# Optimization experiments

Measured on AMD Instinct MI355X. Metric: run time of the kernel, lower is better.

## Reference

```python
import jax, jax.numpy as jnp
import numpy as np
from jax import lax

# ---- dims / config (see init_kwargs) ----
M_IMG, N_PCD, C = 1008, 1024, 256     # coarse img nodes (24*32+12*16+6*8), coarse pcd nodes, feat dim
NI_F, NP_F = 76800, 30000             # fine img pixels (240*320), fine pcd points
KI, KP = 64, 64                       # knn patch sizes
NUM_CORR, TOPK = 256, 3               # coarse matching params
COARSE_THR, FINE_THR = 0.0, 0.0       # similarity thresholds (lowered for random data)


def _norm(x):
    return x / (jnp.linalg.norm(x, axis=-1, keepdims=True) + 1e-8)


def setup_inputs() -> dict:
    key = jax.random.key(0)
    ks = jax.random.split(key, 7)
    return {
        "img_feats_c": _norm(jax.random.normal(ks[0], (M_IMG, C), jnp.float32)),
        "pcd_feats_c": _norm(jax.random.normal(ks[1], (N_PCD, C), jnp.float32)),
        "img_feats_f": _norm(jax.random.normal(ks[2], (NI_F, C), jnp.float32)),
        "pcd_feats_f": _norm(jax.random.normal(ks[3], (NP_F, C), jnp.float32)),
        "img_node_masks": jnp.ones((M_IMG,), bool),
        "pcd_node_masks": jnp.ones((N_PCD,), bool),
        "img_node_knn_indices": jax.random.randint(ks[4], (M_IMG, KI), 0, NI_F),
        "pcd_node_knn_indices": jax.random.randint(ks[5], (N_PCD, KP), 0, NP_F),
        "pcd_node_knn_masks": jax.random.uniform(ks[6], (N_PCD, KP)) > 0.1,
    }


def _coarse_match(img_feats_c, pcd_feats_c, img_masks, pcd_masks):
    # SuperPointMatchingMutualTopk: cosine sim + mutual top-k + global top NUM_CORR
    sim = img_feats_c @ pcd_feats_c.T                              # [M, N] (feats normalized)
    valid = img_masks[:, None] & pcd_masks[None, :]
    sim_m = jnp.where(valid, sim, -jnp.inf)
    row_kth = lax.top_k(sim_m, TOPK)[0][:, -1:]                    # kth-largest per row [M,1]
    col_kth = lax.top_k(sim_m.T, TOPK)[0][:, -1:].T                # kth-largest per col [1,N]
    mutual = (sim_m >= row_kth) & (sim_m >= col_kth) & (sim_m > COARSE_THR)
    flat = jnp.where(mutual, sim_m, -jnp.inf).ravel()
    vals, flat_idx = lax.top_k(flat, NUM_CORR)                     # fixed-size selection
    img_idx = flat_idx // N_PCD
    pcd_idx = flat_idx % N_PCD
    corr_valid = jnp.isfinite(vals)
    return img_idx, pcd_idx, corr_valid


def reference(img_feats_c, pcd_feats_c, img_feats_f, pcd_feats_f,
              img_node_masks, pcd_node_masks,
              img_node_knn_indices, pcd_node_knn_indices, pcd_node_knn_masks):
    # ---- coarse matching ----
    img_idx, pcd_idx, corr_valid = _coarse_match(
        img_feats_c, pcd_feats_c, img_node_masks, pcd_node_masks)

    # ---- fine matching: knn gather + pairwise cosine + mutual top-1 ----
    pcd_padded = jnp.concatenate([pcd_feats_f, jnp.zeros_like(pcd_feats_f[:1])], axis=0)
    img_knn_idx = img_node_knn_indices[img_idx]                    # [Ci, KI]
    pcd_knn_idx = pcd_node_knn_indices[pcd_idx]                    # [Ci, KP]
    pcd_knn_msk = pcd_node_knn_masks[pcd_idx]                      # [Ci, KP]
    img_knn_feats = img_feats_f[img_knn_idx]                       # [Ci, KI, C]
    pcd_knn_feats = pcd_padded[pcd_knn_idx]                        # [Ci, KP, C]

    sim = jnp.einsum('bic,bjc->bij', img_knn_feats, pcd_knn_feats) # [Ci, KI, KP]
    m3 = corr_valid[:, None, None] & pcd_knn_msk[:, None, :]
    sim = jnp.where(m3, sim, -jnp.inf)

    row_best = jnp.argmax(sim, axis=2)                             # [Ci, KI]
    row_val = jnp.max(sim, axis=2)
    col_best = jnp.argmax(sim, axis=1)                             # [Ci, KP]
    back = jnp.take_along_axis(col_best, row_best, axis=1)         # [Ci, KI]
    sel = (back == jnp.arange(KI)[None, :]) & jnp.isfinite(row_val) & (row_val > FINE_THR)

    img_corr = img_knn_idx.reshape(-1)                             # [Ci*KI]
    pcd_corr = jnp.take_along_axis(pcd_knn_idx, row_best, axis=1).reshape(-1)
    sel = sel.reshape(-1)
    # sentinel for unselected pairs -> sorts last
    img_corr = jnp.where(sel, img_corr, NI_F)
    pcd_corr = jnp.where(sel, pcd_corr, NP_F)

    # ---- dedup (torch.unique on img*Npf+pcd) via lexsort + first-occurrence mask ----
    order = jnp.lexsort((pcd_corr, img_corr))
    ic, pc = img_corr[order], pcd_corr[order]
    first = jnp.concatenate([jnp.array([True]),
                             (ic[1:] != ic[:-1]) | (pc[1:] != pc[:-1])])
    valid = first & (ic < NI_F)

    ic_s = jnp.clip(ic, 0, NI_F - 1)
    pc_s = jnp.clip(pc, 0, NP_F - 1)
    corr_scores = jnp.sum(img_feats_f[ic_s] * pcd_feats_f[pc_s], axis=1)
    corr_scores = corr_scores * valid.astype(corr_scores.dtype)    # masked scores [Ci*KI]
    return corr_scores
```

## Files before the change

### kernel.cpp

```cpp
#include <hip/hip_runtime.h>
#include <hip/hip_bf16.h>

#define M_IMG 1008
#define N_PCD 1024
#define CDIM  256
#define NI_F  76800
#define NP_F  30000
#define KI    64
#define KP    64
#define NUM_CORR 256
#define NPAIR (NUM_CORR * KI)
#define CAND_CAP 4096
#define KEY_MOD 30001u
#define SENT_KEY (76800u * 30001u + 30000u)

#define NCHUNK 21
#define NEG_INF (-__builtin_inff())

__device__ __forceinline__ bool mask_val(const void* p, int i, int is_u8) {
    return is_u8 ? (((const unsigned char*)p)[i] != 0)
                 : (((const int*)p)[i] != 0);
}

__global__ void detect_bool_kernel(const unsigned int* __restrict__ p,
                                   int* __restrict__ flag) {
    __shared__ int s_cnt;
    if (threadIdx.x == 0) s_cnt = 0;
    __syncthreads();
    unsigned int x = p[blockIdx.x * 256 + threadIdx.x];
    if (x & 0xFFFFFF00u) atomicAdd(&s_cnt, 1);
    __syncthreads();
    if (threadIdx.x == 0 && s_cnt != 0) atomicAdd(flag, 1);
}


__global__ void coarse_sim_kernel(const float* __restrict__ A,
                                  const float* __restrict__ B,
                                  const void* __restrict__ maskA,
                                  const void* __restrict__ maskB,
                                  const int* __restrict__ flag,
                                  float* __restrict__ sim) {
    __shared__ __align__(16) float s_a[32][36];
    __shared__ __align__(16) float s_b[32][68];
    const int is_u8 = (*flag != 0);
    const int m0 = blockIdx.y * 32, n0 = blockIdx.x * 64;
    const int tid = threadIdx.x;
    const int tx = tid & 15, ty = tid >> 4;
    const int c_lane = tid & 31;
    const int r_base = tid >> 5;

    const float* pa[4];
    const float* pb[8];
#pragma unroll
    for (int k = 0; k < 4; k++) {
        int m = m0 + r_base + 8 * k;
        pa[k] = A + (size_t)(m < M_IMG ? m : 0) * CDIM + c_lane;
    }
#pragma unroll
    for (int k = 0; k < 8; k++)
        pb[k] = B + (size_t)(n0 + r_base + 8 * k) * CDIM + c_lane;

    float ra[4], rb[8];
#pragma unroll
    for (int k = 0; k < 4; k++) ra[k] = pa[k][0];
#pragma unroll
    for (int k = 0; k < 8; k++) rb[k] = pb[k][0];
#pragma unroll
    for (int k = 0; k < 4; k++) s_a[c_lane][r_base + 8 * k] = ra[k];
#pragma unroll
    for (int k = 0; k < 8; k++) s_b[c_lane][r_base + 8 * k] = rb[k];
    __syncthreads();

    float acc[2][4];
#pragma unroll
    for (int r = 0; r < 2; r++)
#pragma unroll
        for (int j = 0; j < 4; j++) acc[r][j] = 0.f;

    for (int cit = 0; cit < 8; cit++) {
        if (cit < 7) {
            const int cc = (cit + 1) * 32;
#pragma unroll
            for (int k = 0; k < 4; k++) ra[k] = pa[k][cc];
#pragma unroll
            for (int k = 0; k < 8; k++) rb[k] = pb[k][cc];
        }
#pragma unroll 8
        for (int c = 0; c < 32; c++) {
            float2 av = *(const float2*)&s_a[c][ty * 2];
            float4 bv = *(const float4*)&s_b[c][tx * 4];
            float ar[2] = {av.x, av.y};
            float br[4] = {bv.x, bv.y, bv.z, bv.w};
#pragma unroll
            for (int r = 0; r < 2; r++)
#pragma unroll
                for (int j = 0; j < 4; j++) acc[r][j] += ar[r] * br[j];
        }
        __syncthreads();
        if (cit < 7) {
#pragma unroll
            for (int k = 0; k < 4; k++) s_a[c_lane][r_base + 8 * k] = ra[k];
#pragma unroll
            for (int k = 0; k < 8; k++) s_b[c_lane][r_base + 8 * k] = rb[k];
            __syncthreads();
        }
    }
#pragma unroll
    for (int r = 0; r < 2; r++) {
        int m = m0 + ty * 2 + r;
        if (m < M_IMG) {
            bool ma = mask_val(maskA, m, is_u8);
#pragma unroll
            for (int j = 0; j < 4; j++) {
                int n = n0 + tx * 4 + j;
                bool ok = ma && mask_val(maskB, n, is_u8);
                sim[m * N_PCD + n] = ok ? acc[r][j] : NEG_INF;
            }
        }
    }
}

__device__ __forceinline__ void top3_insert(float v, float& t0, float& t1, float& t2) {
    if (v > t0) { t2 = t1; t1 = t0; t0 = v; }
    else if (v > t1) { t2 = t1; t1 = v; }
    else if (v > t2) { t2 = v; }
}

__device__ __forceinline__ void top3_merge(float a0, float a1, float a2,
                                           float b0, float b1, float b2,
                                           float& x0, float& x1, float& x2) {
    if (a0 >= b0) {
        x0 = a0;
        if (a1 >= b0) { x1 = a1; x2 = (a2 >= b0) ? a2 : b0; }
        else          { x1 = b0; x2 = (a1 >= b1) ? a1 : b1; }
    } else {
        x0 = b0;
        if (b1 >= a0) { x1 = b1; x2 = (b2 >= a0) ? b2 : a0; }
        else          { x1 = a0; x2 = (b1 >= a1) ? b1 : a1; }
    }
}

__global__ void kth_kernel(const float* __restrict__ sim,
                           float* __restrict__ row_kth,
                           float* __restrict__ colp) {
    __shared__ float st[256][3];
    const int tid = threadIdx.x;
    if (blockIdx.x < M_IMG) {
        const float* r = sim + (size_t)blockIdx.x * N_PCD;
        float t0 = NEG_INF, t1 = NEG_INF, t2 = NEG_INF;
#pragma unroll
        for (int e = 0; e < 4; e++) top3_insert(r[e * 256 + tid], t0, t1, t2);
        st[tid][0] = t0; st[tid][1] = t1; st[tid][2] = t2;
        __syncthreads();
        for (int s = 128; s > 0; s >>= 1) {
            if (tid < s) {
                float x0, x1, x2;
                top3_merge(st[tid][0], st[tid][1], st[tid][2],
                           st[tid + s][0], st[tid + s][1], st[tid + s][2],
                           x0, x1, x2);
                st[tid][0] = x0; st[tid][1] = x1; st[tid][2] = x2;
            }
            __syncthreads();
        }
        if (tid == 0) row_kth[blockIdx.x] = st[0][2];
    } else {
        const int b = blockIdx.x - M_IMG;
        const int bx = b & 15, by = b >> 4;
        const int c = tid & 63, rr = tid >> 6;
        const int col = bx * 64 + c;
        const int r0 = by * 48;
        float t0 = NEG_INF, t1 = NEG_INF, t2 = NEG_INF;
#pragma unroll
        for (int k = 0; k < 12; k++) {
            float v = sim[(size_t)(r0 + rr + 4 * k) * N_PCD + col];
            top3_insert(v, t0, t1, t2);
        }
        st[tid][0] = t0; st[tid][1] = t1; st[tid][2] = t2;
        __syncthreads();
        if (tid < 128) {
            float x0, x1, x2;
            top3_merge(st[tid][0], st[tid][1], st[tid][2],
                       st[tid + 128][0], st[tid + 128][1], st[tid + 128][2],
                       x0, x1, x2);
            st[tid][0] = x0; st[tid][1] = x1; st[tid][2] = x2;
        }
        __syncthreads();
        if (tid < 64) {
            float x0, x1, x2;
            top3_merge(st[tid][0], st[tid][1], st[tid][2],
                       st[tid + 64][0], st[tid + 64][1], st[tid + 64][2],
                       x0, x1, x2);
            const int base = by * N_PCD + col;
            colp[base] = x0;
            colp[NCHUNK * N_PCD + base] = x1;
            colp[2 * NCHUNK * N_PCD + base] = x2;
        }
    }
}

__global__ void col_merge_kernel(const float* __restrict__ colp,
                                 float* __restrict__ col_kth) {
    const int col = blockIdx.x * 256 + threadIdx.x;
    float t0 = colp[col];
    float t1 = colp[NCHUNK * N_PCD + col];
    float t2 = colp[2 * NCHUNK * N_PCD + col];
#pragma unroll
    for (int ch = 1; ch < NCHUNK; ch++) {
        float b0 = colp[ch * N_PCD + col];
        float b1 = colp[NCHUNK * N_PCD + ch * N_PCD + col];
        float b2 = colp[2 * NCHUNK * N_PCD + ch * N_PCD + col];
        float x0, x1, x2;
        top3_merge(t0, t1, t2, b0, b1, b2, x0, x1, x2);
        t0 = x0; t1 = x1; t2 = x2;
    }
    col_kth[col] = t2;
}

__global__ void compact_kernel(const float* __restrict__ sim,
                               const float* __restrict__ row_kth,
                               const float* __restrict__ col_kth,
                               unsigned long long* __restrict__ cand,
                               int* __restrict__ count) {
    int g = blockIdx.x * 256 + threadIdx.x;
    if (g >= M_IMG * N_PCD) return;
    int m = g >> 10, n = g & 1023;
    float v = sim[g];
    if (v > 0.f && v >= row_kth[m] && v >= col_kth[n]) {
        int pos = atomicAdd(count, 1);
        if (pos < CAND_CAP) {
            unsigned int u = __float_as_uint(v);
            unsigned int mono = (u & 0x80000000u) ? ~u : (u | 0x80000000u);
            cand[pos] = ((unsigned long long)(~mono) << 32) | (unsigned int)g;
        }
    }
}

__global__ void cand_rank_kernel(const unsigned long long* __restrict__ cand,
                                 const int* __restrict__ count,
                                 unsigned int* __restrict__ cnt2) {
    __shared__ unsigned long long s_k[256];
    const int tid = threadIdx.x;
    int K = *count; if (K > CAND_CAP) K = CAND_CAP;
    const int j0 = blockIdx.y * 256;
    if (j0 >= K) return;
    int j = j0 + tid;
    s_k[tid] = (j < K) ? cand[j] : 0xFFFFFFFFFFFFFFFFull;
    __syncthreads();
    const int i = blockIdx.x * 256 + tid;
    if (i >= K) return;
    const unsigned long long my = cand[i];
    unsigned int less = 0;
#pragma unroll 8
    for (int t = 0; t < 256; t++) less += (s_k[t] < my);
    if (less) atomicAdd(&cnt2[i], less);
}

__global__ void cand_select_kernel(const unsigned long long* __restrict__ cand,
                                   const int* __restrict__ count,
                                   const unsigned int* __restrict__ cnt2,
                                   int* __restrict__ sel_idx,
                                   int* __restrict__ selK) {
    int K = *count; if (K > CAND_CAP) K = CAND_CAP;
    const int i = blockIdx.x * 256 + threadIdx.x;
    if (i == 0) *selK = (K < NUM_CORR) ? K : NUM_CORR;
    if (i < K) {
        unsigned int r = cnt2[i];
        if (r < NUM_CORR) sel_idx[r] = (int)(cand[i] & 0xFFFFFFFFull);
    }
}

__global__ void fine_kernel(const float* __restrict__ img_f,
                            const float* __restrict__ pcd_f,
                            const int* __restrict__ img_knn,
                            const int* __restrict__ pcd_knn,
                            const void* __restrict__ pcd_msk,
                            const int* __restrict__ flag,
                            const int* __restrict__ sel_idx,
                            const int* __restrict__ selK_ptr,
                            unsigned int* __restrict__ keys) {
    const int ci = blockIdx.x, tid = threadIdx.x;
    const int selK = *selK_ptr;
    if (ci >= selK) {
        if (tid < KI) keys[ci * KI + tid] = SENT_KEY;
        return;
    }
    __shared__ int s_ik[KI], s_pk[KP];
    __shared__ unsigned char s_mk[KP];
    __shared__ __align__(16) float s_a[32][68];
    __shared__ __align__(16) float s_b[32][68];
    __shared__ float s_sim[64][65];
    __shared__ int s_rb[64], s_cb[64];
    __shared__ float s_rv[64];

    int flat = sel_idx[ci];
    int gi = flat >> 10, pi = flat & 1023;
    if (tid < 64) {
        const int is_u8 = (*flag != 0);
        s_ik[tid] = img_knn[gi * KI + tid];
        s_pk[tid] = pcd_knn[pi * KP + tid];
        s_mk[tid] = mask_val(pcd_msk, pi * KP + tid, is_u8) ? 1 : 0;
    }
    __syncthreads();

    const int tx = tid & 15, tyy = tid >> 4;
    const int c_lane = tid & 31;
    const int r_base = tid >> 5;

    const float* pa[4];
    const float* pb[4];
#pragma unroll
    for (int k = 0; k < 4; k++) {
        pa[k] = img_f + (size_t)s_ik[r_base + 16 * k] * CDIM + c_lane;
        pb[k] = pcd_f + (size_t)s_pk[r_base + 16 * k] * CDIM + c_lane;
    }

    float ra[4], rb[4];
#pragma unroll
    for (int k = 0; k < 4; k++) { ra[k] = pa[k][0]; rb[k] = pb[k][0]; }
#pragma unroll
    for (int k = 0; k < 4; k++) {
        s_a[c_lane][r_base + 16 * k] = ra[k];
        s_b[c_lane][r_base + 16 * k] = rb[k];
    }
    __syncthreads();

    float acc[2][4];
#pragma unroll
    for (int r = 0; r < 2; r++)
#pragma unroll
        for (int j = 0; j < 4; j++) acc[r][j] = 0.f;

    for (int cit = 0; cit < 8; cit++) {
        if (cit < 7) {
            const int cc = (cit + 1) * 32;
#pragma unroll
            for (int k = 0; k < 4; k++) { ra[k] = pa[k][cc]; rb[k] = pb[k][cc]; }
        }
#pragma unroll 8
        for (int c = 0; c < 32; c++) {
            float2 av = *(const float2*)&s_a[c][tyy * 2];
            float4 bv = *(const float4*)&s_b[c][tx * 4];
            float ar[2] = {av.x, av.y};
            float br[4] = {bv.x, bv.y, bv.z, bv.w};
#pragma unroll
            for (int r = 0; r < 2; r++)
#pragma unroll
                for (int j = 0; j < 4; j++) acc[r][j] += ar[r] * br[j];
        }
        __syncthreads();
        if (cit < 7) {
#pragma unroll
            for (int k = 0; k < 4; k++) {
                s_a[c_lane][r_base + 16 * k] = ra[k];
                s_b[c_lane][r_base + 16 * k] = rb[k];
            }
            __syncthreads();
        }
    }
#pragma unroll
    for (int r = 0; r < 2; r++) {
        int row = tyy * 2 + r;
#pragma unroll
        for (int j = 0; j < 4; j++) {
            int kp = tx * 4 + j;
            s_sim[row][kp] = (s_mk[kp] != 0) ? acc[r][j] : NEG_INF;
        }
    }
    __syncthreads();

    if (tid < 64) {
        float best = NEG_INF; int bi = 0;
        for (int kp = 0; kp < 64; kp++) {
            float v = s_sim[tid][kp];
            if (v > best) { best = v; bi = kp; }
        }
        s_rb[tid] = bi; s_rv[tid] = best;
    } else if (tid < 128) {
        int kp = tid - 64;
        float best = NEG_INF; int bi = 0;
        for (int k2 = 0; k2 < 64; k2++) {
            float v = s_sim[k2][kp];
            if (v > best) { best = v; bi = k2; }
        }
        s_cb[kp] = bi;
    }
    __syncthreads();

    if (tid < 64) {
        int rb2 = s_rb[tid];
        float rv = s_rv[tid];
        bool sel = (s_cb[rb2] == tid) && (rv > 0.f);
        unsigned int key = sel
            ? ((unsigned int)s_ik[tid] * KEY_MOD + (unsigned int)s_pk[rb2])
            : SENT_KEY;
        keys[ci * KI + tid] = key;
    }
}

__global__ void rank_count_kernel(const unsigned int* __restrict__ keys,
                                  unsigned int* __restrict__ cnt) {
    __shared__ unsigned int s_k[256];
    const int tid = threadIdx.x;
    const int bi = blockIdx.x, bj = blockIdx.y;
    const int i = bi * 256 + tid;
    const unsigned int myKey = keys[i];
    s_k[tid] = keys[bj * 256 + tid];
    __syncthreads();

    unsigned int less = 0, eqb = 0;
    if (bj < bi) {
#pragma unroll 8
        for (int j = 0; j < 256; j++) {
            unsigned int k = s_k[j];
            less += (k < myKey);
            eqb += (k == myKey);
        }
    } else if (bj == bi) {
#pragma unroll 8
        for (int j = 0; j < 256; j++) {
            unsigned int k = s_k[j];
            less += (k < myKey);
            eqb += (k == myKey) & (j < tid);
        }
    } else {
#pragma unroll 8
        for (int j = 0; j < 256; j++) {
            unsigned int k = s_k[j];
            less += (k < myKey);
        }
    }
    atomicAdd(&cnt[i], (less << 16) | eqb);
}

__global__ void rank_out_kernel(const unsigned int* __restrict__ keys,
                                const unsigned int* __restrict__ cnt,
                                const float* __restrict__ img_f,
                                const float* __restrict__ pcd_f,
                                float* __restrict__ out) {
    const int i = blockIdx.x * 256 + threadIdx.x;
    const unsigned int myKey = keys[i];
    const unsigned int v = cnt[i];
    const int rank = (int)(v >> 16) + (int)(v & 0xFFFFu);
    unsigned int ic = myKey / KEY_MOD;
    unsigned int pc = myKey - ic * KEY_MOD;
    float score = 0.f;
    if ((v & 0xFFFFu) == 0 && ic < (unsigned)NI_F) {
        const float4* a = (const float4*)(img_f + (size_t)ic * CDIM);
        const float4* b = (const float4*)(pcd_f + (size_t)pc * CDIM);
        float s = 0.f;
#pragma unroll 8
        for (int c = 0; c < CDIM / 4; c++) {
            float4 x = a[c], y = b[c];
            s += x.x * y.x + x.y * y.y + x.z * y.z + x.w * y.w;
        }
        score = s;
    }
    out[rank] = score;
}

extern "C" void kernel_launch(void* const* d_in, const int* in_sizes, int n_in,
                              void* d_out, int out_size, void* d_ws, size_t ws_size,
                              hipStream_t stream) {
    const float* img_c = (const float*)d_in[0];
    const float* pcd_c = (const float*)d_in[1];
    const float* img_f = (const float*)d_in[2];
    const float* pcd_f = (const float*)d_in[3];
    const void* img_mask = d_in[4];
    const void* pcd_mask = d_in[5];
    const int* img_knn = (const int*)d_in[6];
    const int* pcd_knn = (const int*)d_in[7];
    const void* pcd_knn_msk = d_in[8];
    float* out = (float*)d_out;

    char* w = (char*)d_ws;
    size_t off = 0;
    float* sim = (float*)(w + off);            off += (size_t)M_IMG * N_PCD * 4;
    float* row_kth = (float*)(w + off);        off += M_IMG * 4;
    float* col_kth = (float*)(w + off);        off += N_PCD * 4;
    int* count = (int*)(w + off);              off += 4;
    int* selK = (int*)(w + off);               off += 4;
    int* boolflag = (int*)(w + off);           off += 4;
    off = (off + 7) & ~(size_t)7;
    unsigned long long* cand = (unsigned long long*)(w + off); off += CAND_CAP * 8;
    int* sel_idx = (int*)(w + off);            off += NUM_CORR * 4;
    unsigned int* keys = (unsigned int*)(w + off); off += NPAIR * 4;
    unsigned int* cnt = (unsigned int*)(w + off);  off += NPAIR * 4;
    unsigned int* cnt2 = (unsigned int*)(w + off); off += CAND_CAP * 4;
    float* colp = (float*)(w + off);           off += 3 * NCHUNK * N_PCD * 4;

    hipMemsetAsync(count, 0, 12, stream);
    hipMemsetAsync(cnt, 0, (NPAIR + CAND_CAP) * 4, stream);

    detect_bool_kernel<<<16, 256, 0, stream>>>((const unsigned int*)pcd_knn_msk, boolflag);
    coarse_sim_kernel<<<dim3(16, 32), 256, 0, stream>>>(img_c, pcd_c, img_mask, pcd_mask,
                                                        boolflag, sim);
    kth_kernel<<<M_IMG + 16 * NCHUNK, 256, 0, stream>>>(sim, row_kth, colp);
    col_merge_kernel<<<4, 256, 0, stream>>>(colp, col_kth);
    compact_kernel<<<(M_IMG * N_PCD) / 256, 256, 0, stream>>>(sim, row_kth, col_kth, cand, count);
    cand_rank_kernel<<<dim3(16, 16), 256, 0, stream>>>(cand, count, cnt2);
    cand_select_kernel<<<16, 256, 0, stream>>>(cand, count, cnt2, sel_idx, selK);
    fine_kernel<<<NUM_CORR, 512, 0, stream>>>(img_f, pcd_f, img_knn, pcd_knn, pcd_knn_msk,
                                              boolflag, sel_idx, selK, keys);
    rank_count_kernel<<<dim3(64, 64), 256, 0, stream>>>(keys, cnt);
    rank_out_kernel<<<NPAIR / 256, 256, 0, stream>>>(keys, cnt, img_f, pcd_f, out);
}
```

Baseline: 275.8 us.

## Collapse coarse/fine selection pipeline into fewer kernels with compacted keys

Removes the mask-detect kernel and memsets by folding bool detection and output zeroing into the coarse similarity kernel. Row top-3 now tracks indices, so the mutual check only scans 3 candidates per row instead of the whole similarity matrix. Column merge, candidate compaction and selection are fused into a single-block bitonic sort. Fine matches are compacted via an atomic counter, and one rank kernel computes ranks only over the valid keys, replacing the dense 16K x 16K rank count. The trade-off is a serial single-block sort stage and atomic ordering nondeterminism in the key list.

```diff
diff --git a/kernel.cpp b/kernel.cpp
--- a/kernel.cpp
+++ b/kernel.cpp
@@ -1,5 +1,4 @@
 #include <hip/hip_runtime.h>
-#include <hip/hip_bf16.h>
 
 #define M_IMG 1008
 #define N_PCD 1024
@@ -10,114 +9,14 @@
 #define KP    64
 #define NUM_CORR 256
 #define NPAIR (NUM_CORR * KI)
-#define CAND_CAP 4096
 #define KEY_MOD 30001u
-#define SENT_KEY (76800u * 30001u + 30000u)
-
 #define NCHUNK 21
+#define SORT_N 4096
 #define NEG_INF (-__builtin_inff())
 
 __device__ __forceinline__ bool mask_val(const void* p, int i, int is_u8) {
     return is_u8 ? (((const unsigned char*)p)[i] != 0)
                  : (((const int*)p)[i] != 0);
-}
-
-__global__ void detect_bool_kernel(const unsigned int* __restrict__ p,
-                                   int* __restrict__ flag) {
-    __shared__ int s_cnt;
-    if (threadIdx.x == 0) s_cnt = 0;
-    __syncthreads();
-    unsigned int x = p[blockIdx.x * 256 + threadIdx.x];
-    if (x & 0xFFFFFF00u) atomicAdd(&s_cnt, 1);
-    __syncthreads();
-    if (threadIdx.x == 0 && s_cnt != 0) atomicAdd(flag, 1);
-}
-
-
-__global__ void coarse_sim_kernel(const float* __restrict__ A,
-                                  const float* __restrict__ B,
-                                  const void* __restrict__ maskA,
-                                  const void* __restrict__ maskB,
-                                  const int* __restrict__ flag,
-                                  float* __restrict__ sim) {
-    __shared__ __align__(16) float s_a[32][36];
-    __shared__ __align__(16) float s_b[32][68];
-    const int is_u8 = (*flag != 0);
-    const int m0 = blockIdx.y * 32, n0 = blockIdx.x * 64;
-    const int tid = threadIdx.x;
-    const int tx = tid & 15, ty = tid >> 4;
-    const int c_lane = tid & 31;
-    const int r_base = tid >> 5;
-
-    const float* pa[4];
-    const float* pb[8];
-#pragma unroll
-    for (int k = 0; k < 4; k++) {
-        int m = m0 + r_base + 8 * k;
-        pa[k] = A + (size_t)(m < M_IMG ? m : 0) * CDIM + c_lane;
-    }
-#pragma unroll
-    for (int k = 0; k < 8; k++)
-        pb[k] = B + (size_t)(n0 + r_base + 8 * k) * CDIM + c_lane;
-
-    float ra[4], rb[8];
-#pragma unroll
-    for (int k = 0; k < 4; k++) ra[k] = pa[k][0];
-#pragma unroll
-    for (int k = 0; k < 8; k++) rb[k] = pb[k][0];
-#pragma unroll
-    for (int k = 0; k < 4; k++) s_a[c_lane][r_base + 8 * k] = ra[k];
-#pragma unroll
-    for (int k = 0; k < 8; k++) s_b[c_lane][r_base + 8 * k] = rb[k];
-    __syncthreads();
-
-    float acc[2][4];
-#pragma unroll
-    for (int r = 0; r < 2; r++)
-#pragma unroll
-        for (int j = 0; j < 4; j++) acc[r][j] = 0.f;
-
-    for (int cit = 0; cit < 8; cit++) {
-        if (cit < 7) {
-            const int cc = (cit + 1) * 32;
-#pragma unroll
-            for (int k = 0; k < 4; k++) ra[k] = pa[k][cc];
-#pragma unroll
-            for (int k = 0; k < 8; k++) rb[k] = pb[k][cc];
-        }
-#pragma unroll 8
-        for (int c = 0; c < 32; c++) {
-            float2 av = *(const float2*)&s_a[c][ty * 2];
-            float4 bv = *(const float4*)&s_b[c][tx * 4];
-            float ar[2] = {av.x, av.y};
-            float br[4] = {bv.x, bv.y, bv.z, bv.w};
-#pragma unroll
-            for (int r = 0; r < 2; r++)
-#pragma unroll
-                for (int j = 0; j < 4; j++) acc[r][j] += ar[r] * br[j];
-        }
-        __syncthreads();
-        if (cit < 7) {
-#pragma unroll
-            for (int k = 0; k < 4; k++) s_a[c_lane][r_base + 8 * k] = ra[k];
-#pragma unroll
-            for (int k = 0; k < 8; k++) s_b[c_lane][r_base + 8 * k] = rb[k];
-            __syncthreads();
-        }
-    }
-#pragma unroll
-    for (int r = 0; r < 2; r++) {
-        int m = m0 + ty * 2 + r;
-        if (m < M_IMG) {
-            bool ma = mask_val(maskA, m, is_u8);
-#pragma unroll
-            for (int j = 0; j < 4; j++) {
-                int n = n0 + tx * 4 + j;
-                bool ok = ma && mask_val(maskB, n, is_u8);
-                sim[m * N_PCD + n] = ok ? acc[r][j] : NEG_INF;
-            }
-        }
-    }
 }
 
 __device__ __forceinline__ void top3_insert(float v, float& t0, float& t1, float& t2) {
@@ -140,29 +39,146 @@
     }
 }
 
+__device__ __forceinline__ void t3i_insert(float v, int i,
+                                           float& v0, int& i0,
+                                           float& v1, int& i1,
+                                           float& v2, int& i2) {
+    if (v > v0) { v2 = v1; i2 = i1; v1 = v0; i1 = i0; v0 = v; i0 = i; }
+    else if (v > v1) { v2 = v1; i2 = i1; v1 = v; i1 = i; }
+    else if (v > v2) { v2 = v; i2 = i; }
+}
+
+__global__ void coarse_sim_kernel(const float* __restrict__ A,
+                                  const float* __restrict__ B,
+                                  const void* __restrict__ maskA,
+                                  const void* __restrict__ maskB,
+                                  const unsigned int* __restrict__ mskw,
+                                  float* __restrict__ sim,
+                                  float* __restrict__ out0,
+                                  int* __restrict__ nk) {
+    __shared__ __align__(16) float s_a[32][36];
+    __shared__ __align__(16) float s_b[32][68];
+    const int m0 = blockIdx.y * 32, n0 = blockIdx.x * 64;
+    const int tid = threadIdx.x;
+    const int tx = tid & 15, ty = tid >> 4;
+    const int c_lane = tid & 31;
+    const int r_base = tid >> 5;
+
+    const int bid = blockIdx.y * 16 + blockIdx.x;
+    if (tid < 32) out0[bid * 32 + tid] = 0.f;
+    if (bid == 0 && tid == 32) *nk = 0;
+
+    const bool hit = (mskw[tid] & 0xFFFFFF00u) != 0u;
+
+    const float* pa[4];
+    const float* pb[8];
+#pragma unroll
+    for (int k = 0; k < 4; k++) {
+        int m = m0 + r_base + 8 * k;
+        pa[k] = A + (size_t)(m < M_IMG ? m : 0) * CDIM + c_lane;
+    }
+#pragma unroll
+    for (int k = 0; k < 8; k++)
+        pb[k] = B + (size_t)(n0 + r_base + 8 * k) * CDIM + c_lane;
+
+    float ra[4], rb[8];
+#pragma unroll
+    for (int k = 0; k < 4; k++) ra[k] = pa[k][0];
+#pragma unroll
+    for (int k = 0; k < 8; k++) rb[k] = pb[k][0];
+#pragma unroll
+    for (int k = 0; k < 4; k++) s_a[c_lane][r_base + 8 * k] = ra[k];
+#pragma unroll
+    for (int k = 0; k < 8; k++) s_b[c_lane][r_base + 8 * k] = rb[k];
+    __syncthreads();
+
+    float acc[2][4];
+#pragma unroll
+    for (int r = 0; r < 2; r++)
+#pragma unroll
+        for (int j = 0; j < 4; j++) acc[r][j] = 0.f;
+
+    for (int cit = 0; cit < 8; cit++) {
+        if (cit < 7) {
+            const int cc = (cit + 1) * 32;
+#pragma unroll
+            for (int k = 0; k < 4; k++) ra[k] = pa[k][cc];
+#pragma unroll
+            for (int k = 0; k < 8; k++) rb[k] = pb[k][cc];
+        }
+#pragma unroll 8
+        for (int c = 0; c < 32; c++) {
+            float2 av = *(const float2*)&s_a[c][ty * 2];
+            float4 bv = *(const float4*)&s_b[c][tx * 4];
+            float ar[2] = {av.x, av.y};
+            float br[4] = {bv.x, bv.y, bv.z, bv.w};
+#pragma unroll
+            for (int r = 0; r < 2; r++)
+#pragma unroll
+                for (int j = 0; j < 4; j++) acc[r][j] += ar[r] * br[j];
+        }
+        __syncthreads();
+        if (cit < 7) {
+#pragma unroll
+            for (int k = 0; k < 4; k++) s_a[c_lane][r_base + 8 * k] = ra[k];
+#pragma unroll
+            for (int k = 0; k < 8; k++) s_b[c_lane][r_base + 8 * k] = rb[k];
+            __syncthreads();
+        }
+    }
+
+    const int is_u8 = __syncthreads_or(hit ? 1 : 0);
+#pragma unroll
+    for (int r = 0; r < 2; r++) {
+        int m = m0 + ty * 2 + r;
+        if (m < M_IMG) {
+            bool ma = mask_val(maskA, m, is_u8);
+#pragma unroll
+            for (int j = 0; j < 4; j++) {
+                int n = n0 + tx * 4 + j;
+                bool ok = ma && mask_val(maskB, n, is_u8);
+                sim[m * N_PCD + n] = ok ? acc[r][j] : NEG_INF;
+            }
+        }
+    }
+}
+
 __global__ void kth_kernel(const float* __restrict__ sim,
-                           float* __restrict__ row_kth,
+                           float* __restrict__ rowv3,
+                           int* __restrict__ rowi3,
                            float* __restrict__ colp) {
-    __shared__ float st[256][3];
+    __shared__ float sv[256][3];
+    __shared__ int   si[256][3];
     const int tid = threadIdx.x;
     if (blockIdx.x < M_IMG) {
         const float* r = sim + (size_t)blockIdx.x * N_PCD;
-        float t0 = NEG_INF, t1 = NEG_INF, t2 = NEG_INF;
-#pragma unroll
-        for (int e = 0; e < 4; e++) top3_insert(r[e * 256 + tid], t0, t1, t2);
-        st[tid][0] = t0; st[tid][1] = t1; st[tid][2] = t2;
+        float v0 = NEG_INF, v1 = NEG_INF, v2 = NEG_INF;
+        int i0 = 0, i1 = 0, i2 = 0;
+#pragma unroll
+        for (int e = 0; e < 4; e++) {
+            int c = e * 256 + tid;
+            t3i_insert(r[c], c, v0, i0, v1, i1, v2, i2);
+        }
+        sv[tid][0] = v0; sv[tid][1] = v1; sv[tid][2] = v2;
+        si[tid][0] = i0; si[tid][1] = i1; si[tid][2] = i2;
         __syncthreads();
         for (int s = 128; s > 0; s >>= 1) {
             if (tid < s) {
-                float x0, x1, x2;
-                top3_merge(st[tid][0], st[tid][1], st[tid][2],
-                           st[tid + s][0], st[tid + s][1], st[tid + s][2],
-                           x0, x1, x2);
-                st[tid][0] = x0; st[tid][1] = x1; st[tid][2] = x2;
+                float a0 = sv[tid][0], a1 = sv[tid][1], a2 = sv[tid][2];
+                int   j0 = si[tid][0], j1 = si[tid][1], j2 = si[tid][2];
+#pragma unroll
+                for (int k = 0; k < 3; k++)
+                    t3i_insert(sv[tid + s][k], si[tid + s][k],
+                               a0, j0, a1, j1, a2, j2);
+                sv[tid][0] = a0; sv[tid][1] = a1; sv[tid][2] = a2;
+                si[tid][0] = j0; si[tid][1] = j1; si[tid][2] = j2;
             }
             __syncthreads();
         }
-        if (tid == 0) row_kth[blockIdx.x] = st[0][2];
+        if (tid < 3) {
+            rowv3[blockIdx.x * 3 + tid] = sv[0][tid];
+            rowi3[blockIdx.x * 3 + tid] = si[0][tid];
+        }
     } else {
         const int b = blockIdx.x - M_IMG;
         const int bx = b & 15, by = b >> 4;
@@ -175,20 +191,20 @@
             float v = sim[(size_t)(r0 + rr + 4 * k) * N_PCD + col];
             top3_insert(v, t0, t1, t2);
         }
-        st[tid][0] = t0; st[tid][1] = t1; st[tid][2] = t2;
+        sv[tid][0] = t0; sv[tid][1] = t1; sv[tid][2] = t2;
         __syncthreads();
         if (tid < 128) {
             float x0, x1, x2;
-            top3_merge(st[tid][0], st[tid][1], st[tid][2],
-                       st[tid + 128][0], st[tid + 128][1], st[tid + 128][2],
+            top3_merge(sv[tid][0], sv[tid][1], sv[tid][2],
+                       sv[tid + 128][0], sv[tid + 128][1], sv[tid + 128][2],
                        x0, x1, x2);
-            st[tid][0] = x0; st[tid][1] = x1; st[tid][2] = x2;
+            sv[tid][0] = x0; sv[tid][1] = x1; sv[tid][2] = x2;
         }
         __syncthreads();
         if (tid < 64) {
             float x0, x1, x2;
-            top3_merge(st[tid][0], st[tid][1], st[tid][2],
-                       st[tid + 64][0], st[tid + 64][1], st[tid + 64][2],
+            top3_merge(sv[tid][0], sv[tid][1], sv[tid][2],
+                       sv[tid + 64][0], sv[tid + 64][1], sv[tid + 64][2],
                        x0, x1, x2);
             const int base = by * N_PCD + col;
             colp[base] = x0;
@@ -198,75 +214,68 @@
     }
 }
 
-__global__ void col_merge_kernel(const float* __restrict__ colp,
-                                 float* __restrict__ col_kth) {
-    const int col = blockIdx.x * 256 + threadIdx.x;
-    float t0 = colp[col];
-    float t1 = colp[NCHUNK * N_PCD + col];
-    float t2 = colp[2 * NCHUNK * N_PCD + col];
-#pragma unroll
-    for (int ch = 1; ch < NCHUNK; ch++) {
-        float b0 = colp[ch * N_PCD + col];
-        float b1 = colp[NCHUNK * N_PCD + ch * N_PCD + col];
-        float b2 = colp[2 * NCHUNK * N_PCD + ch * N_PCD + col];
-        float x0, x1, x2;
-        top3_merge(t0, t1, t2, b0, b1, b2, x0, x1, x2);
-        t0 = x0; t1 = x1; t2 = x2;
-    }
-    col_kth[col] = t2;
-}
-
-__global__ void compact_kernel(const float* __restrict__ sim,
-                               const float* __restrict__ row_kth,
-                               const float* __restrict__ col_kth,
-                               unsigned long long* __restrict__ cand,
-                               int* __restrict__ count) {
-    int g = blockIdx.x * 256 + threadIdx.x;
-    if (g >= M_IMG * N_PCD) return;
-    int m = g >> 10, n = g & 1023;
-    float v = sim[g];
-    if (v > 0.f && v >= row_kth[m] && v >= col_kth[n]) {
-        int pos = atomicAdd(count, 1);
-        if (pos < CAND_CAP) {
+__global__ __launch_bounds__(1024)
+void merge_select_kernel(const float* __restrict__ colp,
+                         const float* __restrict__ rowv3,
+                         const int* __restrict__ rowi3,
+                         int* __restrict__ sel_idx,
+                         int* __restrict__ selK) {
+    __shared__ float s_colk[N_PCD];
+    __shared__ __align__(16) unsigned long long s_cand[SORT_N];
+    __shared__ int s_cnt;
+    const int tid = threadIdx.x;
+
+    {
+        float t0 = colp[tid];
+        float t1 = colp[NCHUNK * N_PCD + tid];
+        float t2 = colp[2 * NCHUNK * N_PCD + tid];
+#pragma unroll 4
+        for (int ch = 1; ch < NCHUNK; ch++) {
+            float b0 = colp[ch * N_PCD + tid];
+            float b1 = colp[NCHUNK * N_PCD + ch * N_PCD + tid];
+            float b2 = colp[2 * NCHUNK * N_PCD + ch * N_PCD + tid];
+            float x0, x1, x2;
+            top3_merge(t0, t1, t2, b0, b1, b2, x0, x1, x2);
+            t0 = x0; t1 = x1; t2 = x2;
+        }
+        s_colk[tid] = t2;
+    }
+    if (tid == 0) s_cnt = 0;
+    for (int i = tid; i < SORT_N; i += 1024) s_cand[i] = ~0ULL;
+    __syncthreads();
+
+    for (int e = tid; e < M_IMG * 3; e += 1024) {
+        float v = rowv3[e];
+        int n = rowi3[e];
+        if (v > 0.f && v >= s_colk[n]) {
+            int m = e / 3;
+            int g = m * N_PCD + n;
             unsigned int u = __float_as_uint(v);
             unsigned int mono = (u & 0x80000000u) ? ~u : (u | 0x80000000u);
-            cand[pos] = ((unsigned long long)(~mono) << 32) | (unsigned int)g;
-        }
-    }
-}
-
-__global__ void cand_rank_kernel(const unsigned long long* __restrict__ cand,
-                                 const int* __restrict__ count,
-                                 unsigned int* __restrict__ cnt2) {
-    __shared__ unsigned long long s_k[256];
-    const int tid = threadIdx.x;
-    int K = *count; if (K > CAND_CAP) K = CAND_CAP;
-    const int j0 = blockIdx.y * 256;
-    if (j0 >= K) return;
-    int j = j0 + tid;
-    s_k[tid] = (j < K) ? cand[j] : 0xFFFFFFFFFFFFFFFFull;
-    __syncthreads();
-    const int i = blockIdx.x * 256 + tid;
-    if (i >= K) return;
-    const unsigned long long my = cand[i];
-    unsigned int less = 0;
-#pragma unroll 8
-    for (int t = 0; t < 256; t++) less += (s_k[t] < my);
-    if (less) atomicAdd(&cnt2[i], less);
-}
-
-__global__ void cand_select_kernel(const unsigned long long* __restrict__ cand,
-                                   const int* __restrict__ count,
-                                   const unsigned int* __restrict__ cnt2,
-                                   int* __restrict__ sel_idx,
-                                   int* __restrict__ selK) {
-    int K = *count; if (K > CAND_CAP) K = CAND_CAP;
-    const int i = blockIdx.x * 256 + threadIdx.x;
-    if (i == 0) *selK = (K < NUM_CORR) ? K : NUM_CORR;
-    if (i < K) {
-        unsigned int r = cnt2[i];
-        if (r < NUM_CORR) sel_idx[r] = (int)(cand[i] & 0xFFFFFFFFull);
-    }
+            int pos = atomicAdd(&s_cnt, 1);
+            s_cand[pos] = ((unsigned long long)(~mono) << 32) | (unsigned int)g;
+        }
+    }
+    __syncthreads();
+    int K = s_cnt;
+
+    for (int k = 2; k <= SORT_N; k <<= 1) {
+        for (int j = k >> 1; j > 0; j >>= 1) {
+            for (int i = tid; i < SORT_N; i += 1024) {
+                int ixj = i ^ j;
+                if (ixj > i) {
+                    bool up = ((i & k) == 0);
+                    unsigned long long a = s_cand[i], b = s_cand[ixj];
+                    if ((a > b) == up) { s_cand[i] = b; s_cand[ixj] = a; }
+                }
+            }
+            __syncthreads();
+        }
+    }
+
+    if (K > NUM_CORR) K = NUM_CORR;
+    if (tid == 0) *selK = K;
+    if (tid < K) sel_idx[tid] = (int)(s_cand[tid] & 0xFFFFFFFFu);
 }
 
 __global__ void fine_kernel(const float* __restrict__ img_f,
@@ -274,16 +283,13 @@
                             const int* __restrict__ img_knn,
                             const int* __restrict__ pcd_knn,
                             const void* __restrict__ pcd_msk,
-                            const int* __restrict__ flag,
+                            const unsigned int* __restrict__ mskw,
                             const int* __restrict__ sel_idx,
                             const int* __restrict__ selK_ptr,
-                            unsigned int* __restrict__ keys) {
+                            int* __restrict__ nk,
+                            unsigned int* __restrict__ ckeys) {
     const int ci = blockIdx.x, tid = threadIdx.x;
-    const int selK = *selK_ptr;
-    if (ci >= selK) {
-        if (tid < KI) keys[ci * KI + tid] = SENT_KEY;
-        return;
-    }
+    if (ci >= *selK_ptr) return;
     __shared__ int s_ik[KI], s_pk[KP];
     __shared__ unsigned char s_mk[KP];
     __shared__ __align__(16) float s_a[32][68];
@@ -292,15 +298,16 @@
     __shared__ int s_rb[64], s_cb[64];
     __shared__ float s_rv[64];
 
+    const bool hit = (mskw[tid & 255] & 0xFFFFFF00u) != 0u;
     int flat = sel_idx[ci];
     int gi = flat >> 10, pi = flat & 1023;
     if (tid < 64) {
-        const int is_u8 = (*flag != 0);
         s_ik[tid] = img_knn[gi * KI + tid];
         s_pk[tid] = pcd_knn[pi * KP + tid];
+    }
+    const int is_u8 = __syncthreads_or(hit ? 1 : 0);
+    if (tid < 64)
         s_mk[tid] = mask_val(pcd_msk, pi * KP + tid, is_u8) ? 1 : 0;
-    }
-    __syncthreads();
 
     const int tx = tid & 15, tyy = tid >> 4;
     const int c_lane = tid & 31;
@@ -389,62 +396,44 @@
     if (tid < 64) {
         int rb2 = s_rb[tid];
         float rv = s_rv[tid];
-        bool sel = (s_cb[rb2] == tid) && (rv > 0.f);
-        unsigned int key = sel
-            ? ((unsigned int)s_ik[tid] * KEY_MOD + (unsigned int)s_pk[rb2])
-            : SENT_KEY;
-        keys[ci * KI + tid] = key;
-    }
-}
-
-__global__ void rank_count_kernel(const unsigned int* __restrict__ keys,
-                                  unsigned int* __restrict__ cnt) {
+        if ((s_cb[rb2] == tid) && (rv > 0.f)) {
+            unsigned int key = (unsigned int)s_ik[tid] * KEY_MOD
+                             + (unsigned int)s_pk[rb2];
+            int pos = atomicAdd(nk, 1);
+            ckeys[pos] = key;
+        }
+    }
+}
+
+__global__ void rank_kernel(const unsigned int* __restrict__ ckeys,
+                            const int* __restrict__ nk,
+                            const float* __restrict__ img_f,
+                            const float* __restrict__ pcd_f,
+                            float* __restrict__ out) {
     __shared__ unsigned int s_k[256];
-    const int tid = threadIdx.x;
-    const int bi = blockIdx.x, bj = blockIdx.y;
+    const int K = *nk;
+    const int bi = blockIdx.x, tid = threadIdx.x;
+    if (bi * 256 >= K) return;
     const int i = bi * 256 + tid;
-    const unsigned int myKey = keys[i];
-    s_k[tid] = keys[bj * 256 + tid];
-    __syncthreads();
-
-    unsigned int less = 0, eqb = 0;
-    if (bj < bi) {
+    const unsigned int myKey = (i < K) ? ckeys[i] : 0xFFFFFFFFu;
+    int less = 0, eqb = 0;
+    const int nb = (K + 255) >> 8;
+    for (int bj = 0; bj < nb; bj++) {
+        const int j = bj * 256 + tid;
+        s_k[tid] = (j < K) ? ckeys[j] : 0xFFFFFFFFu;
+        __syncthreads();
+        const int jbase = bj * 256;
 #pragma unroll 8
-        for (int j = 0; j < 256; j++) {
-            unsigned int k = s_k[j];
+        for (int t = 0; t < 256; t++) {
+            unsigned int k = s_k[t];
             less += (k < myKey);
-            eqb += (k == myKey);
-        }
-    } else if (bj == bi) {
-#pragma unroll 8
-        for (int j = 0; j < 256; j++) {
-            unsigned int k = s_k[j];
-            less += (k < myKey);
-            eqb += (k == myKey) & (j < tid);
-        }
-    } else {
-#pragma unroll 8
-        for (int j = 0; j < 256; j++) {
-            unsigned int k = s_k[j];
-            less += (k < myKey);
-        }
-    }
-    atomicAdd(&cnt[i], (less << 16) | eqb);
-}
-
-__global__ void rank_out_kernel(const unsigned int* __restrict__ keys,
-                                const unsigned int* __restrict__ cnt,
-                                const float* __restrict__ img_f,
-                                const float* __restrict__ pcd_f,
-                                float* __restrict__ out) {
-    const int i = blockIdx.x * 256 + threadIdx.x;
-    const unsigned int myKey = keys[i];
-    const unsigned int v = cnt[i];
-    const int rank = (int)(v >> 16) + (int)(v & 0xFFFFu);
-    unsigned int ic = myKey / KEY_MOD;
-    unsigned int pc = myKey - ic * KEY_MOD;
-    float score = 0.f;
-    if ((v & 0xFFFFu) == 0 && ic < (unsigned)NI_F) {
+            eqb  += (k == myKey) & ((jbase + t) < i);
+        }
+        __syncthreads();
+    }
+    if (i < K && eqb == 0) {
+        unsigned int ic = myKey / KEY_MOD;
+        unsigned int pc = myKey - ic * KEY_MOD;
         const float4* a = (const float4*)(img_f + (size_t)ic * CDIM);
         const float4* b = (const float4*)(pcd_f + (size_t)pc * CDIM);
         float s = 0.f;
@@ -453,9 +442,8 @@
             float4 x = a[c], y = b[c];
             s += x.x * y.x + x.y * y.y + x.z * y.z + x.w * y.w;
         }
-        score = s;
-    }
-    out[rank] = score;
+        out[less] = s;
+    }
 }
 
 extern "C" void kernel_launch(void* const* d_in, const int* in_sizes, int n_in,
@@ -475,32 +463,22 @@
     char* w = (char*)d_ws;
     size_t off = 0;
     float* sim = (float*)(w + off);            off += (size_t)M_IMG * N_PCD * 4;
-    float* row_kth = (float*)(w + off);        off += M_IMG * 4;
-    float* col_kth = (float*)(w + off);        off += N_PCD * 4;
-    int* count = (int*)(w + off);              off += 4;
+    float* colp = (float*)(w + off);           off += 3 * NCHUNK * N_PCD * 4;
+    float* rowv3 = (float*)(w + off);          off += M_IMG * 3 * 4;
+    int* rowi3 = (int*)(w + off);              off += M_IMG * 3 * 4;
+    int* sel_idx = (int*)(w + off);            off += NUM_CORR * 4;
     int* selK = (int*)(w + off);               off += 4;
-    int* boolflag = (int*)(w + off);           off += 4;
-    off = (off + 7) & ~(size_t)7;
-    unsigned long long* cand = (unsigned long long*)(w + off); off += CAND_CAP * 8;
-    int* sel_idx = (int*)(w + off);            off += NUM_CORR * 4;
-    unsigned int* keys = (unsigned int*)(w + off); off += NPAIR * 4;
-    unsigned int* cnt = (unsigned int*)(w + off);  off += NPAIR * 4;
-    unsigned int* cnt2 = (unsigned int*)(w + off); off += CAND_CAP * 4;
-    float* colp = (float*)(w + off);           off += 3 * NCHUNK * N_PCD * 4;
-
-    hipMemsetAsync(count, 0, 12, stream);
-    hipMemsetAsync(cnt, 0, (NPAIR + CAND_CAP) * 4, stream);
-
-    detect_bool_kernel<<<16, 256, 0, stream>>>((const unsigned int*)pcd_knn_msk, boolflag);
-    coarse_sim_kernel<<<dim3(16, 32), 256, 0, stream>>>(img_c, pcd_c, img_mask, pcd_mask,
-                                                        boolflag, sim);
-    kth_kernel<<<M_IMG + 16 * NCHUNK, 256, 0, stream>>>(sim, row_kth, colp);
-    col_merge_kernel<<<4, 256, 0, stream>>>(colp, col_kth);
-    compact_kernel<<<(M_IMG * N_PCD) / 256, 256, 0, stream>>>(sim, row_kth, col_kth, cand, count);
-    cand_rank_kernel<<<dim3(16, 16), 256, 0, stream>>>(cand, count, cnt2);
-    cand_select_kernel<<<16, 256, 0, stream>>>(cand, count, cnt2, sel_idx, selK);
-    fine_kernel<<<NUM_CORR, 512, 0, stream>>>(img_f, pcd_f, img_knn, pcd_knn, pcd_knn_msk,
-                                              boolflag, sel_idx, selK, keys);
-    rank_count_kernel<<<dim3(64, 64), 256, 0, stream>>>(keys, cnt);
-    rank_out_kernel<<<NPAIR / 256, 256, 0, stream>>>(keys, cnt, img_f, pcd_f, out);
-}
+    int* nk = (int*)(w + off);                 off += 4;
+    unsigned int* ckeys = (unsigned int*)(w + off); off += NPAIR * 4;
+
+    const unsigned int* mskw = (const unsigned int*)pcd_knn_msk;
+
+    coarse_sim_kernel<<<dim3(16, 32), 256, 0, stream>>>(
+        img_c, pcd_c, img_mask, pcd_mask, mskw, sim, out, nk);
+    kth_kernel<<<M_IMG + 16 * NCHUNK, 256, 0, stream>>>(sim, rowv3, rowi3, colp);
+    merge_select_kernel<<<1, 1024, 0, stream>>>(colp, rowv3, rowi3, sel_idx, selK);
+    fine_kernel<<<NUM_CORR, 512, 0, stream>>>(img_f, pcd_f, img_knn, pcd_knn,
+                                              pcd_knn_msk, mskw, sel_idx, selK,
+                                              nk, ckeys);
+    rank_kernel<<<64, 256, 0, stream>>>(ckeys, nk, img_f, pcd_f, out);
+}
```

Result: slower. 469.8 us (+70.4%).
